# Performance work log

Hardware: AMD Instinct MI355X
Metric: run time of the kernel (lower is better)

Reference implementation:

```python
import jax, jax.numpy as jnp
import numpy as np

QLEN, MLEN, BSZ = 1024, 1024, 2
D_MODEL, H, D_HEAD, D_FF = 1024, 16, 64, 4096
KLEN = QLEN + MLEN


def _ln(x, g, b, eps=1e-5):
    mu = jnp.mean(x, axis=-1, keepdims=True)
    var = jnp.var(x, axis=-1, keepdims=True)
    return (x - mu) * jax.lax.rsqrt(var + eps) * g + b


def _rel_shift(x):
    # x: [q, k, b, n] -> Transformer-XL relative shift
    q, k, b, n = x.shape
    zp = jnp.zeros((q, 1, b, n), x.dtype)
    xp = jnp.concatenate([zp, x], axis=1).reshape(k + 1, q, b, n)[1:]
    return xp.reshape(q, k, b, n)


def setup_inputs() -> dict:
    key = jax.random.key(0)
    ks = jax.random.split(key, 12)
    s = 0.02
    inp = {
        "input_": jax.random.normal(ks[0], (QLEN, BSZ, D_MODEL), jnp.float32),
        "mems": jax.random.normal(ks[1], (MLEN, BSZ, D_MODEL), jnp.float32),
        "pos_emb": jax.random.normal(ks[2], (KLEN, 1, D_MODEL), jnp.float32),
        # True = masked. Causal with memory: query i sees keys j <= i + MLEN
        "mask_tgt": jnp.triu(jnp.ones((QLEN, KLEN), bool), k=MLEN + 1),
        "ln1_g": jnp.ones((D_MODEL,), jnp.float32),
        "ln1_b": jnp.zeros((D_MODEL,), jnp.float32),
        "qkv_w": jax.random.normal(ks[3], (D_MODEL, 3 * H * D_HEAD), jnp.float32) * s,
        "qkv_b": jnp.zeros((3 * H * D_HEAD,), jnp.float32),
        "r_w": jax.random.normal(ks[4], (D_MODEL, H * D_HEAD), jnp.float32) * s,
        "r_w_bias": jax.random.normal(ks[5], (H, D_HEAD), jnp.float32) * s,
        "r_r_bias": jax.random.normal(ks[6], (H, D_HEAD), jnp.float32) * s,
        "o_w": jax.random.normal(ks[7], (H * D_HEAD, D_MODEL), jnp.float32) * s,
        "ln2_g": jnp.ones((D_MODEL,), jnp.float32),
        "ln2_b": jnp.zeros((D_MODEL,), jnp.float32),
        "ff_w1": jax.random.normal(ks[8], (D_MODEL, D_FF), jnp.float32) * s,
        "ff_b1": jnp.zeros((D_FF,), jnp.float32),
        "ff_w2": jax.random.normal(ks[9], (D_FF, D_MODEL), jnp.float32) * s,
        "ff_b2": jnp.zeros((D_MODEL,), jnp.float32),
    }
    return inp


def reference(input_, mems, pos_emb, mask_tgt, ln1_g, ln1_b, qkv_w, qkv_b,
              r_w, r_w_bias, r_r_bias, o_w, ln2_g, ln2_b,
              ff_w1, ff_b1, ff_w2, ff_b2):
    qlen, bsz, _ = input_.shape
    # --- pre-norm (applied to both current input and mems) ---
    q_in = _ln(input_, ln1_g, ln1_b)
    m_in = _ln(mems, ln1_g, ln1_b)
    cat = jnp.concatenate([m_in, q_in], axis=0)            # [klen, b, d]
    klen = cat.shape[0]
    heads = cat @ qkv_w + qkv_b                            # [klen, b, 3*h*dh]
    w_q, w_k, w_v = jnp.split(heads, 3, axis=-1)
    w_q = w_q[-qlen:].reshape(qlen, bsz, H, D_HEAD)        # [q, b, h, dh]
    w_k = w_k.reshape(klen, bsz, H, D_HEAD)
    w_v = w_v.reshape(klen, bsz, H, D_HEAD)
    r_k = (pos_emb[:, 0] @ r_w).reshape(klen, H, D_HEAD)   # [k, h, dh]

    AC = jnp.einsum('ibnd,jbnd->ijbn', w_q + r_w_bias, w_k)
    BD = jnp.einsum('ibnd,jnd->ijbn', w_q + r_r_bias, r_k)
    BD = _rel_shift(BD)
    scale = 1.0 / np.sqrt(D_HEAD)
    score = (AC + BD) * scale                              # [q, k, b, h]
    score = jnp.where(mask_tgt[:, :, None, None], -1e30, score)
    prob = jax.nn.softmax(score, axis=1)
    attn = jnp.einsum('ijbn,jbnd->ibnd', prob, w_v).reshape(qlen, bsz, H * D_HEAD)
    attn_out = attn @ o_w                                  # [q, b, d]
    x = input_ + attn_out                                  # residual (dropout = eval)

    # --- FFN block ---
    y = _ln(x, ln2_g, ln2_b)
    y = jax.nn.relu(y @ ff_w1 + ff_b1) @ ff_w2 + ff_b2
    return x + y
```

## Files before the change

kernel.cpp:

```cpp
#include <hip/hip_runtime.h>


typedef unsigned short u16;
typedef unsigned int   u32;
typedef __attribute__((ext_vector_type(8))) short bf16x8;
typedef __attribute__((ext_vector_type(4))) float f32x4;

struct alignas(16) U128 { u32 x[4]; };
struct alignas(16) F128 { float f[4]; };
struct alignas(8)  U64  { u32 x[2]; };

#define DEV static __device__ __forceinline__
#define MF(a, b, c) __builtin_amdgcn_mfma_f32_16x16x32_bf16((a), (b), (c), 0, 0, 0)

typedef __attribute__((address_space(1))) u32 as1_u32;
typedef __attribute__((address_space(3))) u32 as3_u32;
DEV void gload16(const void* g, void* l) {
  __builtin_amdgcn_global_load_lds((as1_u32*)g, (as3_u32*)l, 16, 0, 0);
}

DEV u16 f2bf(float f) {
  union { float f; u32 u; } v; v.f = f;
  u32 r = v.u + 0x7fffu + ((v.u >> 16) & 1u);
  return (u16)(r >> 16);
}
DEV float bf2f(u16 h) {
  union { u32 u; float f; } v; v.u = ((u32)h) << 16;
  return v.f;
}

template <int TWO>
__global__ __launch_bounds__(256) void ln_rows(
    const float* __restrict__ src, const float* __restrict__ src2,
    const float* __restrict__ g, const float* __restrict__ b,
    u16* __restrict__ dst)
{
  int row = blockIdx.x, tid = threadIdx.x;
  const float* s_;
  if constexpr (TWO) s_ = (row < 2048) ? src + (size_t)row * 1024
                                       : src2 + (size_t)(row - 2048) * 1024;
  else s_ = src + (size_t)row * 1024;
  F128 v = ((const F128*)s_)[tid];
  float s = v.f[0] + v.f[1] + v.f[2] + v.f[3];
  float q = v.f[0]*v.f[0] + v.f[1]*v.f[1] + v.f[2]*v.f[2] + v.f[3]*v.f[3];
#pragma unroll
  for (int off = 1; off < 64; off <<= 1) {
    s += __shfl_xor(s, off); q += __shfl_xor(q, off);
  }
  __shared__ float sh[8];
  int wid = tid >> 6;
  if ((tid & 63) == 0) { sh[wid] = s; sh[4 + wid] = q; }
  __syncthreads();
  s = sh[0] + sh[1] + sh[2] + sh[3];
  q = sh[4] + sh[5] + sh[6] + sh[7];
  float mu = s * (1.0f / 1024.0f);
  float rs = rsqrtf(q * (1.0f / 1024.0f) - mu * mu + 1e-5f);
  F128 g4 = ((const F128*)g)[tid];
  F128 b4 = ((const F128*)b)[tid];
  union { u16 h[4]; U64 u; } o;
#pragma unroll
  for (int j = 0; j < 4; j++)
    o.h[j] = f2bf((v.f[j] - mu) * rs * g4.f[j] + b4.f[j]);
  *(U64*)(dst + (size_t)row * 1024 + tid * 4) = o.u;
}

__global__ __launch_bounds__(256) void transpose_w(
    const float* __restrict__ W, u16* __restrict__ Wt, int K, int N)
{
  __shared__ float t[64][65];
  int k0 = blockIdx.x * 64, n0 = blockIdx.y * 64;
  int tid = threadIdx.x;
  int r = tid >> 6, c = tid & 63;
#pragma unroll
  for (int i = 0; i < 16; i++)
    t[r + i * 4][c] = W[(size_t)(k0 + r + i * 4) * N + n0 + c];
  __syncthreads();
#pragma unroll
  for (int i = 0; i < 16; i++) {
    int n = r + i * 4;
    Wt[(size_t)(n0 + n) * K + k0 + c] = f2bf(t[c][n]);
  }
}

__global__ __launch_bounds__(256) void cvt_bf16(
    const float* __restrict__ s, u16* __restrict__ d, int n4)
{
  int i = blockIdx.x * 256 + threadIdx.x;
  if (i >= n4) return;
  F128 v = ((const F128*)s)[i];
  union { u16 h[4]; U64 u; } o;
#pragma unroll
  for (int j = 0; j < 4; j++) o.h[j] = f2bf(v.f[j]);
  ((U64*)d)[i] = o.u;
}

template <int EPI, int NSPLIT>
__global__ __launch_bounds__(256, 2) void gemm_bt(
    const u16* __restrict__ A, const u16* __restrict__ Bt,
    u16* __restrict__ outb, const float* __restrict__ bias,
    float* __restrict__ p0, float* __restrict__ p1,
    float* __restrict__ p2, float* __restrict__ p3,
    int M, int N, int K)
{
  __shared__ u16 As[2][128 * 64];
  __shared__ u16 Bs[2][128 * 64];
  int tid = threadIdx.x;
  int m0 = blockIdx.x * 128, n0 = blockIdx.y * 128;
  int lane = tid & 63, wid = tid >> 6;
  int wr = wid >> 1, wc = wid & 1;
  f32x4 acc[4][4] = {};

  const int Kc = K / NSPLIT;
  const int kbase = (NSPLIT > 1) ? (int)blockIdx.z * Kc : 0;

  const int lrow = wid * 8 + (lane >> 3);
  const int lcol = (lane & 7) * 8;
  const u16* Ag = A  + (size_t)(m0 + lrow) * K + kbase + lcol;
  const u16* Bg = Bt + (size_t)(n0 + lrow) * K + kbase + lcol;

  auto stage = [&](int buf, int k0) {
#pragma unroll
    for (int i = 0; i < 4; i++) {
      gload16(Ag + (size_t)i * 32 * K + k0, &As[buf][(i * 4 + wid) * 512]);
      gload16(Bg + (size_t)i * 32 * K + k0, &Bs[buf][(i * 4 + wid) * 512]);
    }
  };

  stage(0, 0);
  __syncthreads();
  int cur = 0;
  for (int k0 = 0; k0 < Kc; k0 += 64) {
    if (k0 + 64 < Kc) stage(cur ^ 1, k0 + 64);
    bf16x8 af[2][4], bfr[2][4];
#pragma unroll
    for (int kc = 0; kc < 2; kc++)
#pragma unroll
      for (int f = 0; f < 4; f++) {
        af[kc][f]  = *(const bf16x8*)&As[cur][(wr * 64 + f * 16 + (lane & 15)) * 64 + kc * 32 + (lane >> 4) * 8];
        bfr[kc][f] = *(const bf16x8*)&Bs[cur][(wc * 64 + f * 16 + (lane & 15)) * 64 + kc * 32 + (lane >> 4) * 8];
      }
    __builtin_amdgcn_s_setprio(1);
#pragma unroll
    for (int kc = 0; kc < 2; kc++)
#pragma unroll
      for (int fi = 0; fi < 4; fi++)
#pragma unroll
        for (int fj = 0; fj < 4; fj++)
          acc[fi][fj] = MF(af[kc][fi], bfr[kc][fj], acc[fi][fj]);
    __builtin_amdgcn_s_setprio(0);
    __syncthreads();
    cur ^= 1;
  }

  float* part = nullptr;
  if constexpr (NSPLIT > 1) {
    part = (blockIdx.z == 0) ? p0 : (blockIdx.z == 1) ? p1
         : (blockIdx.z == 2) ? p2 : p3;
  }
#pragma unroll
  for (int fi = 0; fi < 4; fi++)
#pragma unroll
    for (int fj = 0; fj < 4; fj++) {
      int col = n0 + wc * 64 + fj * 16 + (lane & 15);
      float bvv = (NSPLIT == 1 && bias != nullptr) ? bias[col] : 0.0f;
#pragma unroll
      for (int r = 0; r < 4; r++) {
        int row = m0 + wr * 64 + fi * 16 + (lane >> 4) * 4 + r;
        float v = acc[fi][fj][r] + bvv;
        if constexpr (NSPLIT > 1) {
          part[(size_t)row * N + col] = v;
        } else {
          if constexpr (EPI == 1) v = fmaxf(v, 0.0f);
          outb[(size_t)row * N + col] = f2bf(v);
        }
      }
    }
}

template <int NS, int EPI>
__global__ __launch_bounds__(256) void reduce_split(
    const float* __restrict__ p0, const float* __restrict__ p1,
    const float* __restrict__ p2, const float* __restrict__ p3,
    const float* __restrict__ bias, const float* __restrict__ resid,
    u16* __restrict__ outb, float* __restrict__ outf, int N)
{
  int e = (blockIdx.x * 256 + threadIdx.x) * 4;
  F128 a = *(const F128*)(p0 + e);
  F128 b = *(const F128*)(p1 + e);
  float v[4];
#pragma unroll
  for (int j = 0; j < 4; j++) v[j] = a.f[j] + b.f[j];
  if constexpr (NS == 4) {
    F128 c = *(const F128*)(p2 + e);
    F128 d = *(const F128*)(p3 + e);
#pragma unroll
    for (int j = 0; j < 4; j++) v[j] += c.f[j] + d.f[j];
  }
  if constexpr (EPI == 2) {
    F128 rv = *(const F128*)(resid + e);
    int col = e % N;
    F128 o;
#pragma unroll
    for (int j = 0; j < 4; j++) {
      float bv = (bias != nullptr) ? bias[col + j] : 0.0f;
      o.f[j] = v[j] + bv + rv.f[j];
    }
    *(F128*)(outf + e) = o;
  } else {
    union { u16 h[4]; U64 u; } o;
#pragma unroll
    for (int j = 0; j < 4; j++) o.h[j] = f2bf(v[j]);
    *(U64*)(outb + e) = o.u;
  }
}

__global__ __launch_bounds__(256) void extract_vt(
    const u16* __restrict__ heads, u16* __restrict__ Vt)
{
  __shared__ u16 t[64][72];
  int jt = blockIdx.x;
  int bh = blockIdx.y;
  int b = bh >> 4, h = bh & 15;
  int tid = threadIdx.x;
  int row = tid >> 2;
  int cc = (tid & 3) * 16;
#pragma unroll
  for (int i = 0; i < 2; i++)
    *(U128*)&t[row][cc + i * 8] =
        *(const U128*)&heads[(size_t)((jt * 64 + row) * 2 + b) * 3072 + 2048 + h * 64 + cc + i * 8];
  __syncthreads();
  int jc = tid & 63, dr = tid >> 6;
#pragma unroll
  for (int i = 0; i < 16; i++) {
    int d = dr + i * 4;
    Vt[((size_t)bh * 64 + d) * 2048 + jt * 64 + jc] = t[jc][d];
  }
}

__global__ __launch_bounds__(256, 2) void attn_fwd(
    const u16* __restrict__ heads, const u16* __restrict__ rk,
    const u16* __restrict__ Vt, const float* __restrict__ rwb,
    const float* __restrict__ rrb, u16* __restrict__ attnout)
{
  __shared__ u16 lds[37376];

  int tid = threadIdx.x, lane = tid & 63, wid = tid >> 6;
  int bh = blockIdx.x;
  int y = (int)blockIdx.y;
  int xt = (y < 8) ? y : 23 - y;
  int i0 = xt * 64;
  int b = bh >> 4, h = bh & 15;

  u16* Ps = lds + 32768;
  u16* Qw = lds;
  u16* Qr = lds + 4608;

  for (int c = tid; c < 512; c += 256) {
    int row = c >> 3, c8 = (c & 7) * 8;
    union { U128 v; u16 h[8]; } in, ow, orr;
    in.v = *(const U128*)&heads[(size_t)((1024 + i0 + row) * 2 + b) * 3072 + h * 64 + c8];
#pragma unroll
    for (int j = 0; j < 8; j++) {
      float q = bf2f(in.h[j]);
      ow.h[j]  = f2bf(q + rwb[h * 64 + c8 + j]);
      orr.h[j] = f2bf(q + rrb[h * 64 + c8 + j]);
    }
    *(U128*)&Qw[row * 72 + c8] = ow.v;
    *(U128*)&Qr[row * 72 + c8] = orr.v;
  }
  __syncthreads();

  bf16x8 qwf[2], qrf[2];
  int qrow = wid * 16 + (lane & 15);
#pragma unroll
  for (int kc = 0; kc < 2; kc++) {
    qwf[kc] = *(const bf16x8*)&Qw[qrow * 72 + kc * 32 + (lane >> 4) * 8];
    qrf[kc] = *(const bf16x8*)&Qr[qrow * 72 + kc * 32 + (lane >> 4) * 8];
  }
  __syncthreads();

  const int srow = lane >> 3;
  const int scol = 8 * ((lane & 7) ^ srow);

  auto stage = [&](int buf, int t) {
    int j0 = t * 64;
    u16* base = lds + buf * 16384;
#pragma unroll
    for (int i = 0; i < 2; i++) {
      int g8 = wid * 2 + i;
      int jr = j0 + g8 * 8 + srow;
      gload16(heads + (size_t)(jr * 2 + b) * 3072 + 1024 + h * 64 + scol,
              base + g8 * 512);
    }
#pragma unroll
    for (int i = 0; i < 2; i++) {
      int g8 = wid * 2 + i;
      int dr = g8 * 8 + srow;
      gload16(Vt + ((size_t)bh * 64 + dr) * 2048 + j0 + scol,
              base + 4096 + g8 * 512);
    }
    int rbase = 960 + j0 - i0;
#pragma unroll
    for (int i = 0; i < 4; i++) {
      int g8 = wid * 4 + i;
      int rr = rbase + g8 * 8 + srow;
      rr = rr < 0 ? 0 : (rr > 2047 ? 2047 : rr);
      gload16(rk + (size_t)rr * 1024 + h * 64 + scol,
              base + 8192 + g8 * 512);
    }
  };

  stage(0, 0);
  __syncthreads();

  float mrow[4], plrow[4];
  f32x4 o[4] = {};
  f32x4 bd[5];
#pragma unroll
  for (int r = 0; r < 4; r++) { mrow[r] = -1e30f; plrow[r] = 0.0f; }

  int nt = i0 / 64 + 17;
  const int roffw = 48 - wid * 16;
  const int g = lane >> 4, cc = lane & 15;
  const int rswz = 8 * (lane & 7);
  const float SCL = 0.18033688f;

  for (int t = 0; t < nt; t++) {
    const u16* base = lds + (t & 1) * 16384;
    if (t + 1 < nt) stage((t + 1) & 1, t + 1);

    const u16* Kb = base;
    const u16* Vb = base + 4096;
    const u16* Rb = base + 8192;

    f32x4 sAC[4] = {};
    if (t == 0) bd[0] = (f32x4){0.f, 0.f, 0.f, 0.f};
#pragma unroll
    for (int fb = 1; fb < 5; fb++) bd[fb] = (f32x4){0.f, 0.f, 0.f, 0.f};
    __builtin_amdgcn_s_setprio(1);
#pragma unroll
    for (int kc = 0; kc < 2; kc++) {
      int cb = (kc * 32 + g * 8) ^ rswz;
#pragma unroll
      for (int fj = 0; fj < 4; fj++) {
        bf16x8 kf = *(const bf16x8*)&Kb[(fj * 16 + (lane & 15)) * 64 + cb];
        sAC[fj] = MF(qwf[kc], kf, sAC[fj]);
      }
      if (t == 0) {
        bf16x8 rf = *(const bf16x8*)&Rb[(roffw + (lane & 15)) * 64 + cb];
        bd[0] = MF(qrf[kc], rf, bd[0]);
      }
#pragma unroll
      for (int fb = 1; fb < 5; fb++) {
        bf16x8 rf = *(const bf16x8*)&Rb[(roffw + fb * 16 + (lane & 15)) * 64 + cb];
        bd[fb] = MF(qrf[kc], rf, bd[fb]);
      }
    }
    __builtin_amdgcn_s_setprio(0);

    float p[4][4];
#pragma unroll
    for (int fj = 0; fj < 4; fj++)
#pragma unroll
      for (int r = 0; r < 4; r++) {
        int sh_ = 15 - 4 * g - r;
        int src = (lane & 48) | ((lane + sh_) & 15);
        float lo = __shfl(bd[fj][r], src);
        float hi = __shfl(bd[fj + 1][r], src);
        float bdv = (cc + sh_ < 16) ? lo : hi;
        p[fj][r] = (sAC[fj][r] + bdv) * SCL;
      }
    bd[0] = bd[4];

    if (t == nt - 1) {
#pragma unroll
      for (int fj = 0; fj < 4; fj++)
#pragma unroll
        for (int r = 0; r < 4; r++)
          if (fj * 16 + cc > 16 * wid + 4 * g + r) p[fj][r] = -1e30f;
    }

    float tmax[4];
#pragma unroll
    for (int r = 0; r < 4; r++)
      tmax[r] = fmaxf(fmaxf(p[0][r], p[1][r]), fmaxf(p[2][r], p[3][r]));

    bool ok = true;
#pragma unroll
    for (int r = 0; r < 4; r++) ok &= (tmax[r] <= mrow[r] + 12.0f);
    if (!__all(ok)) {
#pragma unroll
      for (int off = 1; off < 16; off <<= 1)
#pragma unroll
        for (int r = 0; r < 4; r++)
          tmax[r] = fmaxf(tmax[r], __shfl_xor(tmax[r], off));
#pragma unroll
      for (int r = 0; r < 4; r++) {
        float mn = fmaxf(mrow[r], tmax[r]);
        float ms = exp2f(mrow[r] - mn);
        mrow[r] = mn;
        plrow[r] *= ms;
#pragma unroll
        for (int fd = 0; fd < 4; fd++) o[fd][r] *= ms;
      }
    }

#pragma unroll
    for (int fj = 0; fj < 4; fj++)
#pragma unroll
      for (int r = 0; r < 4; r++) {
        float e = exp2f(p[fj][r] - mrow[r]);
        plrow[r] += e;
        Ps[(wid * 16 + g * 4 + r) * 72 + fj * 16 + cc] = f2bf(e);
      }
    __builtin_amdgcn_s_setprio(1);
#pragma unroll
    for (int kc = 0; kc < 2; kc++) {
      bf16x8 pf = *(const bf16x8*)&Ps[(wid * 16 + (lane & 15)) * 72 + kc * 32 + g * 8];
      int cb = (kc * 32 + g * 8) ^ rswz;
#pragma unroll
      for (int fd = 0; fd < 4; fd++) {
        bf16x8 vf = *(const bf16x8*)&Vb[(fd * 16 + (lane & 15)) * 64 + cb];
        o[fd] = MF(pf, vf, o[fd]);
      }
    }
    __builtin_amdgcn_s_setprio(0);

    __syncthreads();
  }

#pragma unroll
  for (int off = 1; off < 16; off <<= 1)
#pragma unroll
    for (int r = 0; r < 4; r++)
      plrow[r] += __shfl_xor(plrow[r], off);
#pragma unroll
  for (int fd = 0; fd < 4; fd++)
#pragma unroll
    for (int r = 0; r < 4; r++) {
      int ii2 = (lane >> 4) * 4 + r;
      int row = (i0 + wid * 16 + ii2) * 2 + b;
      attnout[(size_t)row * 1024 + h * 64 + fd * 16 + (lane & 15)] = f2bf(o[fd][r] / plrow[r]);
    }
}

extern "C" void kernel_launch(void* const* d_in, const int* in_sizes, int n_in,
                              void* d_out, int out_size, void* d_ws, size_t ws_size,
                              hipStream_t stream)
{
  const float* input_ = (const float*)d_in[0];
  const float* mems   = (const float*)d_in[1];
  const float* pos    = (const float*)d_in[2];
  const float* ln1g = (const float*)d_in[4];
  const float* ln1b = (const float*)d_in[5];
  const float* qkvw = (const float*)d_in[6];
  const float* qkvb = (const float*)d_in[7];
  const float* rw   = (const float*)d_in[8];
  const float* rwb  = (const float*)d_in[9];
  const float* rrb  = (const float*)d_in[10];
  const float* ow   = (const float*)d_in[11];
  const float* ln2g = (const float*)d_in[12];
  const float* ln2b = (const float*)d_in[13];
  const float* fw1  = (const float*)d_in[14];
  const float* fb1  = (const float*)d_in[15];
  const float* fw2  = (const float*)d_in[16];
  const float* fb2  = (const float*)d_in[17];
  float* out = (float*)d_out;

  char* w = (char*)d_ws;
  u16* WT_QKV = (u16*)(w + 0);
  u16* WT_R   = (u16*)(w + 6291456);
  u16* WT_O   = (u16*)(w + 8388608);
  u16* WT_F1  = (u16*)(w + 10485760);
  u16* WT_F2  = (u16*)(w + 18874368);
  u16* POSB   = (u16*)(w + 27262976);
  u16* ATTN   = POSB;
  u16* CATLN  = (u16*)(w + 31457280);
  u16* HEADS  = (u16*)(w + 39845888);
  u16* H1     = HEADS;
  float* X    = (float*)(w + 56623104);
  u16* RK     = (u16*)(w + 65011712);
  u16* VT     = (u16*)(w + 69206016);
  u16* YN     = VT;

  float* RKP0 = (float*)(w + 31457280);
  float* RKP1 = (float*)(w + 69206016);
  float* OWP0 = (float*)(w + 39845888);
  float* OWP1 = (float*)(w + 48234496);
  float* F2P0 = (float*)(w + 0);
  float* F2P1 = (float*)(w + 10485760);
  float* F2P2 = (float*)(w + 31457280);
  float* F2P3 = (float*)(w + 65011712);

  dim3 blk(256);

  transpose_w<<<dim3(16, 48), blk, 0, stream>>>(qkvw, WT_QKV, 1024, 3072);
  transpose_w<<<dim3(16, 16), blk, 0, stream>>>(rw,   WT_R,   1024, 1024);
  transpose_w<<<dim3(16, 16), blk, 0, stream>>>(ow,   WT_O,   1024, 1024);
  transpose_w<<<dim3(16, 64), blk, 0, stream>>>(fw1,  WT_F1,  1024, 4096);
  transpose_w<<<dim3(64, 16), blk, 0, stream>>>(fw2,  WT_F2,  4096, 1024);
  cvt_bf16<<<dim3(2048), blk, 0, stream>>>(pos, POSB, 2048 * 1024 / 4);

  ln_rows<1><<<dim3(4096), blk, 0, stream>>>(mems, input_, ln1g, ln1b, CATLN);

  gemm_bt<0, 1><<<dim3(32, 24), blk, 0, stream>>>(
      CATLN, WT_QKV, HEADS, qkvb, nullptr, nullptr, nullptr, nullptr, 4096, 3072, 1024);
  gemm_bt<0, 2><<<dim3(16, 8, 2), blk, 0, stream>>>(
      POSB, WT_R, nullptr, nullptr, RKP0, RKP1, nullptr, nullptr, 2048, 1024, 1024);
  reduce_split<2, 0><<<dim3(2048), blk, 0, stream>>>(
      RKP0, RKP1, nullptr, nullptr, nullptr, nullptr, RK, nullptr, 1024);

  extract_vt<<<dim3(32, 32), blk, 0, stream>>>(HEADS, VT);
  attn_fwd<<<dim3(32, 16), blk, 0, stream>>>(HEADS, RK, VT, rwb, rrb, ATTN);

  gemm_bt<0, 2><<<dim3(16, 8, 2), blk, 0, stream>>>(
      ATTN, WT_O, nullptr, nullptr, OWP0, OWP1, nullptr, nullptr, 2048, 1024, 1024);
  reduce_split<2, 2><<<dim3(2048), blk, 0, stream>>>(
      OWP0, OWP1, nullptr, nullptr, nullptr, input_, nullptr, X, 1024);

  ln_rows<0><<<dim3(2048), blk, 0, stream>>>(X, nullptr, ln2g, ln2b, YN);
  gemm_bt<1, 1><<<dim3(16, 32), blk, 0, stream>>>(
      YN, WT_F1, H1, fb1, nullptr, nullptr, nullptr, nullptr, 2048, 4096, 1024);
  gemm_bt<0, 4><<<dim3(16, 8, 4), blk, 0, stream>>>(
      H1, WT_F2, nullptr, nullptr, F2P0, F2P1, F2P2, F2P3, 2048, 1024, 4096);
  reduce_split<4, 2><<<dim3(2048), blk, 0, stream>>>(
      F2P0, F2P1, F2P2, F2P3, fb2, X, nullptr, out, 1024);
}
```

Before: 242.5 us.

## Store split-K partials in bf16, fuse O-proj reduce with LN2, restructure attention staging

Split-K GEMM partials are now written in bf16 instead of fp32, halving partial traffic, and the reduce kernels process 8 elements per thread. The O-projection reduction, residual add and second LayerNorm are merged into one kernel, removing a launch and a round trip of X. In attention, the softmax scale is folded into Q, V fragments are loaded directly from global into registers instead of through LDS, the rel-pos keys use a three-slot ring buffer that reuses overlapping rows, and bf16 packing uses v_cvt_pk_bf16_f32. Rounding partials to bf16 before summing adds precision loss.

```diff
diff --git a/kernel.cpp b/kernel.cpp
--- a/kernel.cpp
+++ b/kernel.cpp
@@ -27,6 +27,11 @@
 DEV float bf2f(u16 h) {
   union { u32 u; float f; } v; v.u = ((u32)h) << 16;
   return v.f;
+}
+DEV u32 cvtpk(float lo, float hi) {
+  u32 r;
+  asm("v_cvt_pk_bf16_f32 %0, %1, %2" : "=v"(r) : "v"(lo), "v"(hi));
+  return r;
 }
 
 template <int TWO>
@@ -64,6 +69,48 @@
   *(U64*)(dst + (size_t)row * 1024 + tid * 4) = o.u;
 }
 
+__global__ __launch_bounds__(256) void ln_fuse(
+    const u16* __restrict__ p0, const u16* __restrict__ p1,
+    const float* __restrict__ resid, const float* __restrict__ g,
+    const float* __restrict__ b, float* __restrict__ X, u16* __restrict__ YN)
+{
+  int row = blockIdx.x, tid = threadIdx.x;
+  U64 a = ((const U64*)(p0 + (size_t)row * 1024))[tid];
+  U64 c = ((const U64*)(p1 + (size_t)row * 1024))[tid];
+  F128 rv = ((const F128*)(resid + (size_t)row * 1024))[tid];
+  float x[4];
+  x[0] = bf2f((u16)a.x[0]) + bf2f((u16)c.x[0]) + rv.f[0];
+  x[1] = bf2f((u16)(a.x[0] >> 16)) + bf2f((u16)(c.x[0] >> 16)) + rv.f[1];
+  x[2] = bf2f((u16)a.x[1]) + bf2f((u16)c.x[1]) + rv.f[2];
+  x[3] = bf2f((u16)(a.x[1] >> 16)) + bf2f((u16)(c.x[1] >> 16)) + rv.f[3];
+  F128 xo;
+#pragma unroll
+  for (int j = 0; j < 4; j++) xo.f[j] = x[j];
+  *(F128*)(X + (size_t)row * 1024 + tid * 4) = xo;
+
+  float s = x[0] + x[1] + x[2] + x[3];
+  float q = x[0]*x[0] + x[1]*x[1] + x[2]*x[2] + x[3]*x[3];
+#pragma unroll
+  for (int off = 1; off < 64; off <<= 1) {
+    s += __shfl_xor(s, off); q += __shfl_xor(q, off);
+  }
+  __shared__ float sh[8];
+  int wid = tid >> 6;
+  if ((tid & 63) == 0) { sh[wid] = s; sh[4 + wid] = q; }
+  __syncthreads();
+  s = sh[0] + sh[1] + sh[2] + sh[3];
+  q = sh[4] + sh[5] + sh[6] + sh[7];
+  float mu = s * (1.0f / 1024.0f);
+  float rs = rsqrtf(q * (1.0f / 1024.0f) - mu * mu + 1e-5f);
+  F128 g4 = ((const F128*)g)[tid];
+  F128 b4 = ((const F128*)b)[tid];
+  union { u16 h[4]; U64 u; } o;
+#pragma unroll
+  for (int j = 0; j < 4; j++)
+    o.h[j] = f2bf((x[j] - mu) * rs * g4.f[j] + b4.f[j]);
+  *(U64*)(YN + (size_t)row * 1024 + tid * 4) = o.u;
+}
+
 __global__ __launch_bounds__(256) void transpose_w(
     const float* __restrict__ W, u16* __restrict__ Wt, int K, int N)
 {
@@ -98,8 +145,8 @@
 __global__ __launch_bounds__(256, 2) void gemm_bt(
     const u16* __restrict__ A, const u16* __restrict__ Bt,
     u16* __restrict__ outb, const float* __restrict__ bias,
-    float* __restrict__ p0, float* __restrict__ p1,
-    float* __restrict__ p2, float* __restrict__ p3,
+    u16* __restrict__ p0, u16* __restrict__ p1,
+    u16* __restrict__ p2, u16* __restrict__ p3,
     int M, int N, int K)
 {
   __shared__ u16 As[2][128 * 64];
@@ -152,7 +199,7 @@
     cur ^= 1;
   }
 
-  float* part = nullptr;
+  u16* part = nullptr;
   if constexpr (NSPLIT > 1) {
     part = (blockIdx.z == 0) ? p0 : (blockIdx.z == 1) ? p1
          : (blockIdx.z == 2) ? p2 : p3;
@@ -168,7 +215,7 @@
         int row = m0 + wr * 64 + fi * 16 + (lane >> 4) * 4 + r;
         float v = acc[fi][fj][r] + bvv;
         if constexpr (NSPLIT > 1) {
-          part[(size_t)row * N + col] = v;
+          part[(size_t)row * N + col] = f2bf(v);
         } else {
           if constexpr (EPI == 1) v = fmaxf(v, 0.0f);
           outb[(size_t)row * N + col] = f2bf(v);
@@ -178,39 +225,50 @@
 }
 
 template <int NS, int EPI>
-__global__ __launch_bounds__(256) void reduce_split(
-    const float* __restrict__ p0, const float* __restrict__ p1,
-    const float* __restrict__ p2, const float* __restrict__ p3,
+__global__ __launch_bounds__(256) void reduce_splitb(
+    const u16* __restrict__ p0, const u16* __restrict__ p1,
+    const u16* __restrict__ p2, const u16* __restrict__ p3,
     const float* __restrict__ bias, const float* __restrict__ resid,
     u16* __restrict__ outb, float* __restrict__ outf, int N)
 {
-  int e = (blockIdx.x * 256 + threadIdx.x) * 4;
-  F128 a = *(const F128*)(p0 + e);
-  F128 b = *(const F128*)(p1 + e);
-  float v[4];
-#pragma unroll
-  for (int j = 0; j < 4; j++) v[j] = a.f[j] + b.f[j];
+  int e = (blockIdx.x * 256 + threadIdx.x) * 8;
+  U128 a = *(const U128*)(p0 + e);
+  U128 c = *(const U128*)(p1 + e);
+  float v[8];
+#pragma unroll
+  for (int k = 0; k < 4; k++) {
+    v[2*k]   = bf2f((u16)a.x[k]) + bf2f((u16)c.x[k]);
+    v[2*k+1] = bf2f((u16)(a.x[k] >> 16)) + bf2f((u16)(c.x[k] >> 16));
+  }
   if constexpr (NS == 4) {
-    F128 c = *(const F128*)(p2 + e);
-    F128 d = *(const F128*)(p3 + e);
-#pragma unroll
-    for (int j = 0; j < 4; j++) v[j] += c.f[j] + d.f[j];
+    U128 d2 = *(const U128*)(p2 + e);
+    U128 d3 = *(const U128*)(p3 + e);
+#pragma unroll
+    for (int k = 0; k < 4; k++) {
+      v[2*k]   += bf2f((u16)d2.x[k]) + bf2f((u16)d3.x[k]);
+      v[2*k+1] += bf2f((u16)(d2.x[k] >> 16)) + bf2f((u16)(d3.x[k] >> 16));
+    }
   }
   if constexpr (EPI == 2) {
-    F128 rv = *(const F128*)(resid + e);
+    F128 r0 = *(const F128*)(resid + e);
+    F128 r1 = *(const F128*)(resid + e + 4);
     int col = e % N;
-    F128 o;
+    F128 o0, o1;
 #pragma unroll
     for (int j = 0; j < 4; j++) {
-      float bv = (bias != nullptr) ? bias[col + j] : 0.0f;
-      o.f[j] = v[j] + bv + rv.f[j];
-    }
-    *(F128*)(outf + e) = o;
+      float b0 = (bias != nullptr) ? bias[col + j] : 0.0f;
+      float b1 = (bias != nullptr) ? bias[col + 4 + j] : 0.0f;
+      o0.f[j] = v[j] + b0 + r0.f[j];
+      o1.f[j] = v[4 + j] + b1 + r1.f[j];
+    }
+    *(F128*)(outf + e) = o0;
+    *(F128*)(outf + e + 4) = o1;
   } else {
-    union { u16 h[4]; U64 u; } o;
-#pragma unroll
-    for (int j = 0; j < 4; j++) o.h[j] = f2bf(v[j]);
-    *(U64*)(outb + e) = o.u;
+    U128 o;
+#pragma unroll
+    for (int k = 0; k < 4; k++)
+      o.x[k] = (u32)f2bf(v[2*k]) | ((u32)f2bf(v[2*k+1]) << 16);
+    *(U128*)(outb + e) = o;
   }
 }
 
@@ -242,7 +300,7 @@
     const u16* __restrict__ Vt, const float* __restrict__ rwb,
     const float* __restrict__ rrb, u16* __restrict__ attnout)
 {
-  __shared__ u16 lds[37376];
+  __shared__ u16 lds[25088];
 
   int tid = threadIdx.x, lane = tid & 63, wid = tid >> 6;
   int bh = blockIdx.x;
@@ -250,8 +308,9 @@
   int xt = (y < 8) ? y : 23 - y;
   int i0 = xt * 64;
   int b = bh >> 4, h = bh & 15;
-
-  u16* Ps = lds + 32768;
+  const float SCL = 0.18033688f;
+
+  u16* Ps = lds + 20480;
   u16* Qw = lds;
   u16* Qr = lds + 4608;
 
@@ -262,8 +321,8 @@
 #pragma unroll
     for (int j = 0; j < 8; j++) {
       float q = bf2f(in.h[j]);
-      ow.h[j]  = f2bf(q + rwb[h * 64 + c8 + j]);
-      orr.h[j] = f2bf(q + rrb[h * 64 + c8 + j]);
+      ow.h[j]  = f2bf((q + rwb[h * 64 + c8 + j]) * SCL);
+      orr.h[j] = f2bf((q + rrb[h * 64 + c8 + j]) * SCL);
     }
     *(U128*)&Qw[row * 72 + c8] = ow.v;
     *(U128*)&Qr[row * 72 + c8] = orr.v;
@@ -281,36 +340,33 @@
 
   const int srow = lane >> 3;
   const int scol = 8 * ((lane & 7) ^ srow);
-
-  auto stage = [&](int buf, int t) {
+  const int rbase0 = 960 - i0;
+
+  auto stageK = [&](int buf, int t) {
     int j0 = t * 64;
-    u16* base = lds + buf * 16384;
 #pragma unroll
     for (int i = 0; i < 2; i++) {
       int g8 = wid * 2 + i;
       int jr = j0 + g8 * 8 + srow;
       gload16(heads + (size_t)(jr * 2 + b) * 3072 + 1024 + h * 64 + scol,
-              base + g8 * 512);
-    }
+              lds + buf * 4096 + g8 * 512);
+    }
+  };
+  auto stageR = [&](int absStart) {
+    int slot3 = (absStart >> 6) % 3;
 #pragma unroll
     for (int i = 0; i < 2; i++) {
       int g8 = wid * 2 + i;
-      int dr = g8 * 8 + srow;
-      gload16(Vt + ((size_t)bh * 64 + dr) * 2048 + j0 + scol,
-              base + 4096 + g8 * 512);
-    }
-    int rbase = 960 + j0 - i0;
-#pragma unroll
-    for (int i = 0; i < 4; i++) {
-      int g8 = wid * 4 + i;
-      int rr = rbase + g8 * 8 + srow;
-      rr = rr < 0 ? 0 : (rr > 2047 ? 2047 : rr);
-      gload16(rk + (size_t)rr * 1024 + h * 64 + scol,
-              base + 8192 + g8 * 512);
+      int ar = absStart + g8 * 8 + srow;
+      ar = ar > 2047 ? 2047 : ar;
+      gload16(rk + (size_t)ar * 1024 + h * 64 + scol,
+              lds + 8192 + slot3 * 4096 + g8 * 512);
     }
   };
 
-  stage(0, 0);
+  stageK(0, 0);
+  stageR(rbase0);
+  stageR(rbase0 + 64);
   __syncthreads();
 
   float mrow[4], plrow[4];
@@ -323,16 +379,25 @@
   const int roffw = 48 - wid * 16;
   const int g = lane >> 4, cc = lane & 15;
   const int rswz = 8 * (lane & 7);
-  const float SCL = 0.18033688f;
+  int third = ((rbase0 >> 6)) % 3;
 
   for (int t = 0; t < nt; t++) {
-    const u16* base = lds + (t & 1) * 16384;
-    if (t + 1 < nt) stage((t + 1) & 1, t + 1);
-
-    const u16* Kb = base;
-    const u16* Vb = base + 4096;
-    const u16* Rb = base + 8192;
-
+    int j0 = t * 64;
+    const u16* Kb = lds + (t & 1) * 4096;
+    if (t + 1 < nt) {
+      stageK((t + 1) & 1, t + 1);
+      stageR(rbase0 + 64 * (t + 2));
+    }
+
+    bf16x8 vfr[2][4];
+#pragma unroll
+    for (int kc = 0; kc < 2; kc++)
+#pragma unroll
+      for (int fd = 0; fd < 4; fd++)
+        vfr[kc][fd] = *(const bf16x8*)(Vt + ((size_t)bh * 64 + fd * 16 + cc) * 2048
+                                       + j0 + kc * 32 + g * 8);
+
+    int rowb = third * 64 + roffw + cc;
     f32x4 sAC[4] = {};
     if (t == 0) bd[0] = (f32x4){0.f, 0.f, 0.f, 0.f};
 #pragma unroll
@@ -343,33 +408,37 @@
       int cb = (kc * 32 + g * 8) ^ rswz;
 #pragma unroll
       for (int fj = 0; fj < 4; fj++) {
-        bf16x8 kf = *(const bf16x8*)&Kb[(fj * 16 + (lane & 15)) * 64 + cb];
+        bf16x8 kf = *(const bf16x8*)&Kb[(fj * 16 + cc) * 64 + cb];
         sAC[fj] = MF(qwf[kc], kf, sAC[fj]);
       }
       if (t == 0) {
-        bf16x8 rf = *(const bf16x8*)&Rb[(roffw + (lane & 15)) * 64 + cb];
+        bf16x8 rf = *(const bf16x8*)&lds[8192 + rowb * 64 + cb];
         bd[0] = MF(qrf[kc], rf, bd[0]);
       }
 #pragma unroll
       for (int fb = 1; fb < 5; fb++) {
-        bf16x8 rf = *(const bf16x8*)&Rb[(roffw + fb * 16 + (lane & 15)) * 64 + cb];
+        int rr = rowb + fb * 16;
+        rr -= (rr >= 192) ? 192 : 0;
+        bf16x8 rf = *(const bf16x8*)&lds[8192 + rr * 64 + cb];
         bd[fb] = MF(qrf[kc], rf, bd[fb]);
       }
     }
     __builtin_amdgcn_s_setprio(0);
+    third = (third + 1 == 3) ? 0 : third + 1;
 
     float p[4][4];
 #pragma unroll
-    for (int fj = 0; fj < 4; fj++)
-#pragma unroll
-      for (int r = 0; r < 4; r++) {
-        int sh_ = 15 - 4 * g - r;
-        int src = (lane & 48) | ((lane + sh_) & 15);
-        float lo = __shfl(bd[fj][r], src);
-        float hi = __shfl(bd[fj + 1][r], src);
-        float bdv = (cc + sh_ < 16) ? lo : hi;
-        p[fj][r] = (sAC[fj][r] + bdv) * SCL;
-      }
+    for (int r = 0; r < 4; r++) {
+      int sh_ = 15 - 4 * g - r;
+      int src = (lane & 48) | ((lane + sh_) & 15);
+      float rt[5];
+#pragma unroll
+      for (int fb = 0; fb < 5; fb++) rt[fb] = __shfl(bd[fb][r], src);
+      bool lo = (cc + sh_ < 16);
+#pragma unroll
+      for (int fj = 0; fj < 4; fj++)
+        p[fj][r] = sAC[fj][r] + (lo ? rt[fj] : rt[fj + 1]);
+    }
     bd[0] = bd[4];
 
     if (t == nt - 1) {
@@ -406,23 +475,24 @@
     }
 
 #pragma unroll
-    for (int fj = 0; fj < 4; fj++)
-#pragma unroll
-      for (int r = 0; r < 4; r++) {
-        float e = exp2f(p[fj][r] - mrow[r]);
-        plrow[r] += e;
-        Ps[(wid * 16 + g * 4 + r) * 72 + fj * 16 + cc] = f2bf(e);
-      }
+    for (int r = 0; r < 4; r++) {
+      float e0 = exp2f(p[0][r] - mrow[r]);
+      float e1 = exp2f(p[1][r] - mrow[r]);
+      float e2 = exp2f(p[2][r] - mrow[r]);
+      float e3 = exp2f(p[3][r] - mrow[r]);
+      plrow[r] += (e0 + e1) + (e2 + e3);
+      u32 wA = cvtpk(e0, e1), wB = cvtpk(e2, e3);
+      u16* prow = &Ps[(wid * 16 + g * 4 + r) * 72 + cc];
+      prow[0]  = (u16)wA; prow[16] = (u16)(wA >> 16);
+      prow[32] = (u16)wB; prow[48] = (u16)(wB >> 16);
+    }
     __builtin_amdgcn_s_setprio(1);
 #pragma unroll
     for (int kc = 0; kc < 2; kc++) {
-      bf16x8 pf = *(const bf16x8*)&Ps[(wid * 16 + (lane & 15)) * 72 + kc * 32 + g * 8];
-      int cb = (kc * 32 + g * 8) ^ rswz;
-#pragma unroll
-      for (int fd = 0; fd < 4; fd++) {
-        bf16x8 vf = *(const bf16x8*)&Vb[(fd * 16 + (lane & 15)) * 64 + cb];
-        o[fd] = MF(pf, vf, o[fd]);
-      }
+      bf16x8 pf = *(const bf16x8*)&Ps[(wid * 16 + cc) * 72 + kc * 32 + g * 8];
+#pragma unroll
+      for (int fd = 0; fd < 4; fd++)
+        o[fd] = MF(pf, vfr[kc][fd], o[fd]);
     }
     __builtin_amdgcn_s_setprio(0);
 
@@ -435,13 +505,16 @@
     for (int r = 0; r < 4; r++)
       plrow[r] += __shfl_xor(plrow[r], off);
 #pragma unroll
-  for (int fd = 0; fd < 4; fd++)
-#pragma unroll
-    for (int r = 0; r < 4; r++) {
-      int ii2 = (lane >> 4) * 4 + r;
-      int row = (i0 + wid * 16 + ii2) * 2 + b;
-      attnout[(size_t)row * 1024 + h * 64 + fd * 16 + (lane & 15)] = f2bf(o[fd][r] / plrow[r]);
-    }
+  for (int r = 0; r < 4; r++) {
+    float rl = 1.0f / plrow[r];
+    int ii2 = g * 4 + r;
+    int row = (i0 + wid * 16 + ii2) * 2 + b;
+    u16* orow = attnout + (size_t)row * 1024 + h * 64 + cc;
+    u32 wA = cvtpk(o[0][r] * rl, o[1][r] * rl);
+    u32 wB = cvtpk(o[2][r] * rl, o[3][r] * rl);
+    orow[0]  = (u16)wA; orow[16] = (u16)(wA >> 16);
+    orow[32] = (u16)wB; orow[48] = (u16)(wB >> 16);
+  }
 }
 
 extern "C" void kernel_launch(void* const* d_in, const int* in_sizes, int n_in,
@@ -483,14 +556,14 @@
   u16* VT     = (u16*)(w + 69206016);
   u16* YN     = VT;
 
-  float* RKP0 = (float*)(w + 31457280);
-  float* RKP1 = (float*)(w + 69206016);
-  float* OWP0 = (float*)(w + 39845888);
-  float* OWP1 = (float*)(w + 48234496);
-  float* F2P0 = (float*)(w + 0);
-  float* F2P1 = (float*)(w + 10485760);
-  float* F2P2 = (float*)(w + 31457280);
-  float* F2P3 = (float*)(w + 65011712);
+  u16* RKP0 = (u16*)(w + 31457280);
+  u16* RKP1 = (u16*)(w + 69206016);
+  u16* OWP0 = (u16*)(w + 39845888);
+  u16* OWP1 = (u16*)(w + 44040192);
+  u16* F2P0 = (u16*)(w + 0);
+  u16* F2P1 = (u16*)(w + 10485760);
+  u16* F2P2 = (u16*)(w + 31457280);
+  u16* F2P3 = (u16*)(w + 65011712);
 
   dim3 blk(256);
 
@@ -507,7 +580,7 @@
       CATLN, WT_QKV, HEADS, qkvb, nullptr, nullptr, nullptr, nullptr, 4096, 3072, 1024);
   gemm_bt<0, 2><<<dim3(16, 8, 2), blk, 0, stream>>>(
       POSB, WT_R, nullptr, nullptr, RKP0, RKP1, nullptr, nullptr, 2048, 1024, 1024);
-  reduce_split<2, 0><<<dim3(2048), blk, 0, stream>>>(
+  reduce_splitb<2, 0><<<dim3(1024), blk, 0, stream>>>(
       RKP0, RKP1, nullptr, nullptr, nullptr, nullptr, RK, nullptr, 1024);
 
   extract_vt<<<dim3(32, 32), blk, 0, stream>>>(HEADS, VT);
@@ -515,14 +588,12 @@
 
   gemm_bt<0, 2><<<dim3(16, 8, 2), blk, 0, stream>>>(
       ATTN, WT_O, nullptr, nullptr, OWP0, OWP1, nullptr, nullptr, 2048, 1024, 1024);
-  reduce_split<2, 2><<<dim3(2048), blk, 0, stream>>>(
-      OWP0, OWP1, nullptr, nullptr, nullptr, input_, nullptr, X, 1024);
-
-  ln_rows<0><<<dim3(2048), blk, 0, stream>>>(X, nullptr, ln2g, ln2b, YN);
+  ln_fuse<<<dim3(2048), blk, 0, stream>>>(OWP0, OWP1, input_, ln2g, ln2b, X, YN);
+
   gemm_bt<1, 1><<<dim3(16, 32), blk, 0, stream>>>(
       YN, WT_F1, H1, fb1, nullptr, nullptr, nullptr, nullptr, 2048, 4096, 1024);
   gemm_bt<0, 4><<<dim3(16, 8, 4), blk, 0, stream>>>(
       H1, WT_F2, nullptr, nullptr, F2P0, F2P1, F2P2, F2P3, 2048, 1024, 4096);
-  reduce_split<4, 2><<<dim3(2048), blk, 0, stream>>>(
+  reduce_splitb<4, 2><<<dim3(1024), blk, 0, stream>>>(
       F2P0, F2P1, F2P2, F2P3, fb2, X, nullptr, out, 1024);
 }
```

New measurement: 274.7 us. +13.3%, slower.
